# Performance work log

Hardware: AMD Instinct MI355X
Metric: run time of the kernel (lower is better)

## Reference

```python
import jax, jax.numpy as jnp
import numpy as np

B, V, T = 256, 128000, 16
TOP_K = 100          # min(100, V - n_targets) == 100 since V >> T
TARGET_MARGIN = 1.0
EPS = 1e-8
NEG = -1e30          # sentinel so masked target slots never enter top-k


def setup_inputs() -> dict:
    key = jax.random.key(0)
    k1, k2 = jax.random.split(key)
    # Non-negative sparse activations (SPLADE-style relu output) in [0,1)
    sparse_rep = jax.random.uniform(k1, (B, V), dtype=jnp.float32)
    # Fixed-length padded target id lists (all rows valid -> n_valid = B)
    target_ids = jax.random.randint(k2, (B, T), 0, V).astype(jnp.int64)
    return {"sparse_rep": sparse_rep, "target_ids": target_ids}


def reference(sparse_rep, target_ids):
    # [B, T] gather of target activations (one batched gather, no per-row loop)
    tgt = jnp.take_along_axis(sparse_rep, target_ids, axis=1)
    # -log(a + eps), per-row mean then batch mean == global mean (fixed T)
    target_loss = -jnp.mean(jnp.log(tgt + EPS))
    # hinge margin on target activations
    margin_loss = jnp.mean(jax.nn.relu(TARGET_MARGIN - tgt))
    # mask out target columns per row, then top-k over remaining vocab
    rows = jnp.arange(sparse_rep.shape[0])[:, None]          # [B, 1]
    masked = sparse_rep.at[rows, target_ids].set(NEG)        # [B, V]
    top_vals = jax.lax.top_k(masked, TOP_K)[0]               # [B, TOP_K]
    negative_loss = jnp.mean(top_vals)
    return (target_loss, margin_loss, negative_loss)
```

## Files before the change

### kernel.cpp

```cpp
#include <hip/hip_runtime.h>
#include <cstddef>
#include <cstdint>

#define B_    256
#define V_    128000
#define T_    16
#define TOPK_ 100
#define TPB   1024
#define CAP   4096
#define NF4   (V_ / 4)
#define NHIST 4096

__global__ void zero_out_kernel(float* o) {
    o[0] = 0.f; o[1] = 0.f; o[2] = 0.f;
}

__global__ __launch_bounds__(TPB) void row_kernel(
        const float* __restrict__ sparse,
        const int*   __restrict__ tids,
        float*       __restrict__ out) {
    __shared__ float    s_cand[CAP];
    __shared__ unsigned s_hist[NHIST];
    __shared__ int      s_ids[T_];
    __shared__ int      s_cnt;
    __shared__ int      s_bstar;
    __shared__ float    s_red[128];

    const int row = blockIdx.x;
    const int tid = threadIdx.x;
    const float* __restrict__ rp = sparse + (size_t)row * V_;

    if (tid < T_) s_ids[tid] = tids[row * T_ + tid];
    if (tid == 0) s_cnt = 0;
    __syncthreads();

    if (tid < T_) {
        float x  = rp[s_ids[tid]];
        float tl = -logf(x + 1e-8f);
        float ml = fmaxf(1.0f - x, 0.0f);
        #pragma unroll
        for (int off = 8; off > 0; off >>= 1) {
            tl += __shfl_down(tl, off);
            ml += __shfl_down(ml, off);
        }
        if (tid == 0) {
            atomicAdd(out + 0, tl * (1.0f / (B_ * T_)));
            atomicAdd(out + 1, ml * (1.0f / (B_ * T_)));
        }
    }

    const float4* rp4 = (const float4*)rp;
    const float T0 = 0.996f;
    for (int i = tid; i < NF4; i += TPB) {
        float4 v = rp4[i];
        int col = i << 2;
        float xs[4] = {v.x, v.y, v.z, v.w};
        #pragma unroll
        for (int c = 0; c < 4; ++c) {
            float x = xs[c];
            if (x >= T0) {
                int cc = col + c;
                bool is_t = false;
                #pragma unroll
                for (int j = 0; j < T_; ++j) is_t |= (cc == s_ids[j]);
                if (!is_t) {
                    int k = atomicAdd(&s_cnt, 1);
                    if (k < CAP) s_cand[k] = x;
                }
            }
        }
    }
    __syncthreads();

    int cnt = s_cnt;

    if (cnt < TOPK_ || cnt > CAP) {
        for (int i = tid; i < NHIST; i += TPB) s_hist[i] = 0u;
        __syncthreads();
        for (int i = tid; i < NF4; i += TPB) {
            float4 v = rp4[i];
            float xs[4] = {v.x, v.y, v.z, v.w};
            #pragma unroll
            for (int c = 0; c < 4; ++c) {
                int b = (int)(xs[c] * (float)NHIST);
                b = min(max(b, 0), NHIST - 1);
                atomicAdd(&s_hist[b], 1u);
            }
        }
        __syncthreads();
        if (tid == 0) {
            for (int j = 0; j < T_; ++j) {
                int id = s_ids[j];
                bool dup = false;
                for (int q = 0; q < j; ++q) dup = dup || (s_ids[q] == id);
                if (!dup) {
                    int b = (int)(rp[id] * (float)NHIST);
                    b = min(max(b, 0), NHIST - 1);
                    s_hist[b]--;
                }
            }
            int acc = 0, b = NHIST - 1;
            for (; b >= 0; --b) {
                acc += (int)s_hist[b];
                if (acc >= TOPK_) break;
            }
            s_bstar = max(b, 0);
            s_cnt = 0;
        }
        __syncthreads();
        int bstar = s_bstar;
        for (int i = tid; i < NF4; i += TPB) {
            float4 v = rp4[i];
            int col = i << 2;
            float xs[4] = {v.x, v.y, v.z, v.w};
            #pragma unroll
            for (int c = 0; c < 4; ++c) {
                float x = xs[c];
                int b = (int)(x * (float)NHIST);
                b = min(max(b, 0), NHIST - 1);
                if (b >= bstar) {
                    int cc = col + c;
                    bool is_t = false;
                    #pragma unroll
                    for (int j = 0; j < T_; ++j) is_t |= (cc == s_ids[j]);
                    if (!is_t) {
                        int k = atomicAdd(&s_cnt, 1);
                        if (k < CAP) s_cand[k] = x;
                    }
                }
            }
        }
        __syncthreads();
        cnt = min(s_cnt, CAP);
    }

    int n2 = 128;
    while (n2 < cnt) n2 <<= 1;
    for (int i = cnt + tid; i < n2; i += TPB) s_cand[i] = -1e30f;
    __syncthreads();

    for (int k = 2; k <= n2; k <<= 1) {
        for (int j = k >> 1; j > 0; j >>= 1) {
            for (int i = tid; i < n2; i += TPB) {
                int p = i ^ j;
                if (p > i) {
                    float a = s_cand[i], b = s_cand[p];
                    bool asc = ((i & k) == 0);
                    if (asc ? (a > b) : (a < b)) {
                        s_cand[i] = b; s_cand[p] = a;
                    }
                }
            }
            __syncthreads();
        }
    }

    if (tid < 128) {
        float v = (tid < TOPK_) ? s_cand[n2 - 1 - tid] : 0.f;
        s_red[tid] = v;
    }
    __syncthreads();
    #pragma unroll
    for (int off = 64; off > 0; off >>= 1) {
        if (tid < off) s_red[tid] += s_red[tid + off];
        __syncthreads();
    }
    if (tid == 0) atomicAdd(out + 2, s_red[0] * (1.0f / (B_ * TOPK_)));
}

extern "C" void kernel_launch(void* const* d_in, const int* in_sizes, int n_in,
                              void* d_out, int out_size, void* d_ws, size_t ws_size,
                              hipStream_t stream) {
    const float* sparse = (const float*)d_in[0];
    const int*   tids   = (const int*)d_in[1];
    float*       out    = (float*)d_out;

    zero_out_kernel<<<1, 1, 0, stream>>>(out);
    row_kernel<<<B_, TPB, 0, stream>>>(sparse, tids, out);
}
```

Before: 208.1 us.

## Replace bitonic sort with histogram-based top-k selection and unroll the row scan

Swaps the full bitonic sort of up to 4096 candidates for a second-level 1024-bin histogram over the candidates. Values above the threshold bin are summed directly, and only the boundary bin gets a small serial selection. The row scan is also fully unrolled so each thread issues four float4 loads before processing them, and a max-of-four check skips the per-element threshold tests for most vectors. This cuts the many synchronisation-heavy sort passes and adds memory-level parallelism, at the cost of a serial single-thread fallback when the boundary bin overflows.

```diff
diff --git a/kernel.cpp b/kernel.cpp
--- a/kernel.cpp
+++ b/kernel.cpp
@@ -10,6 +10,9 @@
 #define CAP   4096
 #define NF4   (V_ / 4)
 #define NHIST 4096
+#define NB    1024
+#define BINCAP 256
+#define T0    0.996f
 
 __global__ void zero_out_kernel(float* o) {
     o[0] = 0.f; o[1] = 0.f; o[2] = 0.f;
@@ -21,17 +24,18 @@
         float*       __restrict__ out) {
     __shared__ float    s_cand[CAP];
     __shared__ unsigned s_hist[NHIST];
+    __shared__ unsigned s_chunk[NB / 4];
+    __shared__ float    s_bin[BINCAP];
+    __shared__ float    s_wred[16];
     __shared__ int      s_ids[T_];
-    __shared__ int      s_cnt;
-    __shared__ int      s_bstar;
-    __shared__ float    s_red[128];
+    __shared__ int      s_cnt, s_bq, s_bstar, s_above;
 
     const int row = blockIdx.x;
     const int tid = threadIdx.x;
     const float* __restrict__ rp = sparse + (size_t)row * V_;
 
     if (tid < T_) s_ids[tid] = tids[row * T_ + tid];
-    if (tid == 0) s_cnt = 0;
+    if (tid == 0) { s_cnt = 0; s_bq = 0; }
     __syncthreads();
 
     if (tid < T_) {
@@ -49,30 +53,60 @@
         }
     }
 
-    const float4* rp4 = (const float4*)rp;
-    const float T0 = 0.996f;
-    for (int i = tid; i < NF4; i += TPB) {
-        float4 v = rp4[i];
-        int col = i << 2;
-        float xs[4] = {v.x, v.y, v.z, v.w};
-        #pragma unroll
-        for (int c = 0; c < 4; ++c) {
-            float x = xs[c];
-            if (x >= T0) {
-                int cc = col + c;
-                bool is_t = false;
-                #pragma unroll
-                for (int j = 0; j < T_; ++j) is_t |= (cc == s_ids[j]);
-                if (!is_t) {
-                    int k = atomicAdd(&s_cnt, 1);
-                    if (k < CAP) s_cand[k] = x;
-                }
-            }
-        }
+    const float4* __restrict__ rp4 = (const float4*)rp;
+
+    auto proc = [&](float4 v, int i4) {
+        float mx = fmaxf(fmaxf(v.x, v.y), fmaxf(v.z, v.w));
+        if (mx >= T0) {
+            int col = i4 << 2;
+            float xs[4] = {v.x, v.y, v.z, v.w};
+            #pragma unroll
+            for (int c = 0; c < 4; ++c) {
+                float x = xs[c];
+                if (x >= T0) {
+                    int cc = col + c;
+                    bool is_t = false;
+                    #pragma unroll
+                    for (int j = 0; j < T_; ++j) is_t |= (cc == s_ids[j]);
+                    if (!is_t) {
+                        int k = atomicAdd(&s_cnt, 1);
+                        if (k < CAP) s_cand[k] = x;
+                    }
+                }
+            }
+        }
+    };
+
+    #pragma unroll
+    for (int g = 0; g < 7; ++g) {
+        const int base = g * 4 * TPB + tid;
+        float4 va = rp4[base];
+        float4 vb = rp4[base + TPB];
+        float4 vc = rp4[base + 2 * TPB];
+        float4 vd = rp4[base + 3 * TPB];
+        proc(va, base);
+        proc(vb, base + TPB);
+        proc(vc, base + 2 * TPB);
+        proc(vd, base + 3 * TPB);
+    }
+    {
+        const int base = 28 * TPB + tid;
+        float4 va = rp4[base];
+        float4 vb = rp4[base + TPB];
+        float4 vc = rp4[base + 2 * TPB];
+        proc(va, base);
+        proc(vb, base + TPB);
+        proc(vc, base + 2 * TPB);
+    }
+    if (tid < 256) {
+        const int idx = 31 * TPB + tid;
+        float4 v = rp4[idx];
+        proc(v, idx);
     }
     __syncthreads();
 
     int cnt = s_cnt;
+    float lo = T0;
 
     if (cnt < TOPK_ || cnt > CAP) {
         for (int i = tid; i < NHIST; i += TPB) s_hist[i] = 0u;
@@ -108,7 +142,8 @@
             s_cnt = 0;
         }
         __syncthreads();
-        int bstar = s_bstar;
+        const int bstar = s_bstar;
+        lo = (float)bstar / (float)NHIST;
         for (int i = tid; i < NF4; i += TPB) {
             float4 v = rp4[i];
             int col = i << 2;
@@ -134,38 +169,86 @@
         cnt = min(s_cnt, CAP);
     }
 
-    int n2 = 128;
-    while (n2 < cnt) n2 <<= 1;
-    for (int i = cnt + tid; i < n2; i += TPB) s_cand[i] = -1e30f;
-    __syncthreads();
-
-    for (int k = 2; k <= n2; k <<= 1) {
-        for (int j = k >> 1; j > 0; j >>= 1) {
-            for (int i = tid; i < n2; i += TPB) {
-                int p = i ^ j;
-                if (p > i) {
-                    float a = s_cand[i], b = s_cand[p];
-                    bool asc = ((i & k) == 0);
-                    if (asc ? (a > b) : (a < b)) {
-                        s_cand[i] = b; s_cand[p] = a;
-                    }
-                }
-            }
-            __syncthreads();
-        }
-    }
-
-    if (tid < 128) {
-        float v = (tid < TOPK_) ? s_cand[n2 - 1 - tid] : 0.f;
-        s_red[tid] = v;
-    }
-    __syncthreads();
+    const float scale = (float)NB / (1.0f - lo);
+
+    for (int i = tid; i < NB; i += TPB) s_hist[i] = 0u;
+    __syncthreads();
+
+    for (int i = tid; i < cnt; i += TPB) {
+        int b = (int)((s_cand[i] - lo) * scale);
+        b = min(max(b, 0), NB - 1);
+        atomicAdd(&s_hist[b], 1u);
+    }
+    __syncthreads();
+
+    if (tid < NB / 4) {
+        int base = tid << 2;
+        s_chunk[tid] = s_hist[base] + s_hist[base + 1] +
+                       s_hist[base + 2] + s_hist[base + 3];
+    }
+    __syncthreads();
+
+    if (tid == 0) {
+        int above = 0, bstar = 0;
+        for (int c = (NB >> 2) - 1; c >= 0; --c) {
+            int s = (int)s_chunk[c];
+            if (above + s >= TOPK_) {
+                for (int b = (c << 2) + 3; b >= (c << 2); --b) {
+                    int cb = (int)s_hist[b];
+                    if (above + cb >= TOPK_) { bstar = b; break; }
+                    above += cb;
+                }
+                s_bstar = bstar;
+                s_above = above;
+                break;
+            }
+            above += s;
+        }
+    }
+    __syncthreads();
+
+    const int b2 = s_bstar;
+    float local = 0.f;
+    for (int i = tid; i < cnt; i += TPB) {
+        float v = s_cand[i];
+        int b = (int)((v - lo) * scale);
+        b = min(max(b, 0), NB - 1);
+        if (b > b2) {
+            local += v;
+        } else if (b == b2) {
+            int k = atomicAdd(&s_bq, 1);
+            if (k < BINCAP) s_bin[k] = v;
+        }
+    }
     #pragma unroll
-    for (int off = 64; off > 0; off >>= 1) {
-        if (tid < off) s_red[tid] += s_red[tid + off];
-        __syncthreads();
-    }
-    if (tid == 0) atomicAdd(out + 2, s_red[0] * (1.0f / (B_ * TOPK_)));
+    for (int off = 32; off > 0; off >>= 1) local += __shfl_down(local, off);
+    if ((tid & 63) == 0) s_wred[tid >> 6] = local;
+    __syncthreads();
+
+    if (tid == 0) {
+        float sum = 0.f;
+        #pragma unroll
+        for (int w = 0; w < 16; ++w) sum += s_wred[w];
+        int q = s_bq;
+        int m = TOPK_ - s_above;
+        if (q <= BINCAP) {
+            for (int t = 0; t < m; ++t) {
+                float bv = -1e30f; int bi = 0;
+                for (int i = 0; i < q; ++i)
+                    if (s_bin[i] > bv) { bv = s_bin[i]; bi = i; }
+                sum += bv; s_bin[bi] = -1e30f;
+            }
+        } else {
+            sum = 0.f;
+            for (int t = 0; t < TOPK_; ++t) {
+                float bv = -1e30f; int bi = 0;
+                for (int i = 0; i < cnt; ++i)
+                    if (s_cand[i] > bv) { bv = s_cand[i]; bi = i; }
+                sum += bv; s_cand[bi] = -1e30f;
+            }
+        }
+        atomicAdd(out + 2, sum * (1.0f / (B_ * TOPK_)));
+    }
 }
 
 extern "C" void kernel_launch(void* const* d_in, const int* in_sizes, int n_in,
```

After: 195.5 us. 6.1% less time.
